# Kernel optimization log

Measured on AMD Instinct MI355X. Metric: run time of the kernel, lower is better.

## Reference

```python
import jax, jax.numpy as jnp
import numpy as np


def setup_inputs() -> dict:
    key = jax.random.key(0)
    k1, k2, k3, k4 = jax.random.split(key, 4)
    B, I, P, F = 4096, 1024, 512, 2048
    x = jax.random.normal(k1, (B, I), dtype=jnp.float32)
    # params initialized like torch.rand(...)*2-1 (uniform in [-1,1])
    features = jax.random.uniform(k2, (F, I), dtype=jnp.float32, minval=-1.0, maxval=1.0)
    prototypes = jax.random.uniform(k3, (P, I), dtype=jnp.float32, minval=-1.0, maxval=1.0)
    # scalars: torch inits to zeros; use small nonzero values so output/grads are informative
    abt = jax.random.normal(k4, (3,), dtype=jnp.float32) * 0.1
    alpha = abt[0:1]
    beta = abt[1:2]
    theta = abt[2:3]
    return {"x": x, "features": features, "prototypes": prototypes,
            "alpha": alpha, "beta": beta, "theta": theta}


def reference(x, features, prototypes, alpha, beta, theta):
    # x: [b, i], features: [f, i], prototypes: [p, i]
    # Original einsums broadcast over p but the projection is p-independent:
    xf = x @ features.T            # [b, f]
    pf = prototypes @ features.T   # [p, f]
    x_pres = jax.nn.relu(xf)       # [b, f]
    p_pres = jax.nn.relu(pf)       # [p, f]
    # common[b,p]       = sum_f xf*pf*relu(xf)*relu(pf)
    # x_distinct[b,p]   = sum_f xf*relu(xf)*(1-relu(pf))
    # p_distinct[b,p]   = sum_f pf*relu(pf)*(1-relu(xf))
    a = xf * x_pres                # [b, f]
    c = pf * p_pres                # [p, f]
    common = a @ c.T                                   # [b, p]
    x_distinctive = a @ (1.0 - p_pres).T               # [b, p]
    p_distinctive = (1.0 - x_pres) @ c.T               # [b, p]
    return theta * common - alpha * x_distinctive - beta * p_distinctive
```

## Files before the change

kernel.cpp:

```cpp
#include <hip/hip_runtime.h>
#include <cstdint>

typedef __attribute__((ext_vector_type(8))) short bf16x8;
typedef __attribute__((ext_vector_type(16))) float f32x16;
typedef __attribute__((ext_vector_type(4))) float f4;
typedef __attribute__((ext_vector_type(8))) unsigned short u16x8;
typedef unsigned short u16;


__device__ __forceinline__ u16 f2bf(float f) {
  uint32_t u = __builtin_bit_cast(uint32_t, f);
  u += 0x7fffu + ((u >> 16) & 1u);
  return (u16)(u >> 16);
}

__device__ __forceinline__ float bf2f(u16 h) {
  return __builtin_bit_cast(float, (uint32_t)h << 16);
}

__device__ __forceinline__ void async_cp16(const void* g, void* l) {
  __builtin_amdgcn_global_load_lds(
      (const __attribute__((address_space(1))) uint32_t*)g,
      (__attribute__((address_space(3))) uint32_t*)l, 16, 0, 0);
}

__global__ __launch_bounds__(256) void cast3(
    const float* __restrict__ x, const float* __restrict__ f,
    const float* __restrict__ p, u16* __restrict__ dst,
    int n1, int n2, int n3) {
  int i = (blockIdx.x * 256 + threadIdx.x) * 8;
  const float* src;
  int local;
  if (i < n1) { src = x; local = i; }
  else if (i < n1 + n2) { src = f; local = i - n1; }
  else if (i < n1 + n2 + n3) { src = p; local = i - n1 - n2; }
  else return;
  f4 a = *(const f4*)(src + local);
  f4 b = *(const f4*)(src + local + 4);
  u16x8 o;
  o[0] = f2bf(a.x); o[1] = f2bf(a.y); o[2] = f2bf(a.z); o[3] = f2bf(a.w);
  o[4] = f2bf(b.x); o[5] = f2bf(b.y); o[6] = f2bf(b.z); o[7] = f2bf(b.w);
  *(u16x8*)(dst + i) = o;
}


__device__ __forceinline__ void stage_tile512(
    const u16* __restrict__ A, const u16* __restrict__ B, int K,
    int k0, int tid, u16* L) {
  const int wave = tid >> 6;
  #pragma unroll
  for (int it = 0; it < 2; ++it) {
    int c = it * 512 + tid;
    int row = c >> 3, pc = c & 7;
    int gc = pc ^ (row & 7);
    async_cp16(A + (size_t)row * K + (k0 + gc * 8),
               &L[(it * 512 + wave * 64) * 8]);
  }
  #pragma unroll
  for (int it = 0; it < 2; ++it) {
    int c = it * 512 + tid;
    int row = c >> 3, pc = c & 7;
    int gc = pc ^ (row & 7);
    async_cp16(B + (size_t)row * K + (k0 + gc * 8),
               &L[8192 + (it * 512 + wave * 64) * 8]);
  }
}

__device__ __forceinline__ void compute_tile512(
    const u16* L, int lane, int wrow, int wcol, f32x16 (&acc)[2]) {
  #pragma unroll
  for (int s = 0; s < 4; ++s) {
    const int h = s * 2 + (lane >> 5);
    const int ra = wrow * 32 + (lane & 31);
    bf16x8 afr = *(const bf16x8*)&L[(ra * 8 + (h ^ (ra & 7))) * 8];
    #pragma unroll
    for (int j = 0; j < 2; ++j) {
      const int rb = wcol * 64 + j * 32 + (lane & 31);
      bf16x8 bfr = *(const bf16x8*)&L[8192 + (rb * 8 + (h ^ (rb & 7))) * 8];
      acc[j] = __builtin_amdgcn_mfma_f32_32x32x16_bf16(afr, bfr, acc[j], 0, 0, 0);
    }
  }
}

__device__ __forceinline__ void mainloop512(
    const u16* __restrict__ A, const u16* __restrict__ B, int K,
    int kbeg, int kend, int tid, u16* lds, f32x16 (&acc)[2]) {
  constexpr int BK = 64;
  constexpr int BUF = 16384;
  const int lane = tid & 63;
  const int wave = tid >> 6;
  const int wrow = wave >> 1, wcol = wave & 1;

  stage_tile512(A, B, K, kbeg, tid, lds);
  int cur = 0;
  for (int k0 = kbeg; k0 < kend; k0 += BK) {
    if (k0 + BK < kend) {
      stage_tile512(A, B, K, k0 + BK, tid, lds + (cur ^ 1) * BUF);
      asm volatile("s_waitcnt vmcnt(4)" ::: "memory");
    } else {
      asm volatile("s_waitcnt vmcnt(0)" ::: "memory");
    }
    __builtin_amdgcn_s_barrier();
    compute_tile512(lds + cur * BUF, lane, wrow, wcol, acc);
    __builtin_amdgcn_s_barrier();
    cur ^= 1;
  }
}


__global__ __launch_bounds__(512) void gemm12(
    const u16* __restrict__ xb, const u16* __restrict__ pb,
    const u16* __restrict__ fb, u16* __restrict__ Acat, u16* __restrict__ Bcat,
    const float* __restrict__ alpha, const float* __restrict__ beta,
    const float* __restrict__ theta) {
  constexpr int TM = 128, K = 1024, N = 2048;
  constexpr int TSTRIDE = 136;
  __shared__ u16 lds[32768];

  const int tid = threadIdx.x;
  const int lane = tid & 63;
  const int wave = tid >> 6;
  const int wrow = wave >> 1, wcol = wave & 1;

  const int bid = blockIdx.x;
  const int xcd = bid & 7, slot = bid >> 3;
  const int xt = (xcd & 3) * 9 + (slot >> 3);
  const int yt = (xcd >> 2) * 8 + (slot & 7);

  const int bm_all = xt * TM;
  const int bn = yt * 128;
  const bool is_x = bm_all < 4096;
  const u16* A = is_x ? xb + (size_t)bm_all * K : pb + (size_t)(bm_all - 4096) * K;
  const u16* B = fb + (size_t)bn * K;

  f32x16 acc[2] = {};
  mainloop512(A, B, K, 0, K, tid, lds, acc);

  float th = 0.f, al = 0.f, be = 0.f;
  if (!is_x) { th = theta[0]; al = alpha[0]; be = beta[0]; }
  u16* dst = is_x ? Acat : Bcat;
  const int rowbase = is_x ? bm_all : bm_all - 4096;
  const int rquad = 4 * (lane >> 5);

  #pragma unroll
  for (int half = 0; half < 2; ++half) {
    __syncthreads();
    #pragma unroll
    for (int j = 0; j < 2; ++j) {
      const int cl = wcol * 64 + j * 32 + (lane & 31);
      #pragma unroll
      for (int r = 0; r < 16; ++r) {
        const int rl = wrow * 32 + (r & 3) + 8 * (r >> 2) + rquad;
        float v = acc[j][r];
        float pres = v > 0.f ? v : 0.f;
        float o;
        if (is_x) o = half == 0 ? v * pres : 1.f - pres;
        else {
          float cc = v * pres;
          o = half == 0 ? th * cc - al * (1.f - pres) : -be * cc;
        }
        lds[rl * TSTRIDE + cl] = f2bf(o);
      }
    }
    __syncthreads();
    #pragma unroll
    for (int v = 0; v < 4; ++v) {
      const int rl = v * 32 + (tid >> 4);
      const int c8 = (tid & 15) * 8;
      u16x8 vec = *(const u16x8*)&lds[rl * TSTRIDE + c8];
      *(u16x8*)&dst[(size_t)(rowbase + rl) * (2 * N) + bn + c8 + half * N] = vec;
    }
  }
}

__global__ __launch_bounds__(512) void gemm3(
    const u16* __restrict__ Acat, const u16* __restrict__ Bcat,
    u16* __restrict__ part) {
  constexpr int TM = 128, TN = 128, K = 4096, KSPLIT = 4;
  __shared__ u16 lds[32768];

  const int tid = threadIdx.x;

  const int bid = blockIdx.x;
  const int xcd = bid & 7, slot = bid >> 3;
  const int bz = xcd >> 1;
  const int bxt = (xcd & 1) * 16 + (slot >> 2);
  const int byt = slot & 3;

  const int bm = bxt * TM;
  const int bn = byt * TN;
  const int kbeg = bz * (K / KSPLIT);
  const int kend = kbeg + (K / KSPLIT);

  f32x16 acc[2] = {};
  mainloop512(Acat + (size_t)bm * K, Bcat + (size_t)bn * K, K, kbeg, kend,
              tid, lds, acc);

  const size_t pbase = ((size_t)bz * 128 + byt * 32 + bxt) * 16384;
  #pragma unroll
  for (int j = 0; j < 2; ++j)
    #pragma unroll
    for (int h = 0; h < 2; ++h) {
      u16x8 o;
      #pragma unroll
      for (int e = 0; e < 8; ++e) o[e] = f2bf(acc[j][h * 8 + e]);
      *(u16x8*)&part[pbase + (size_t)(j * 2 + h) * 4096 + tid * 8] = o;
    }
}

__global__ __launch_bounds__(512) void reduce4(
    const u16* __restrict__ part, float* __restrict__ out) {
  constexpr int N = 512;
  const int tid = threadIdx.x;
  const int lane = tid & 63;
  const int wave = tid >> 6;
  const int wrow = wave >> 1, wcol = wave & 1;
  const int tileId = blockIdx.x >> 2;
  const int q = blockIdx.x & 3;
  const int bm = (tileId & 31) * 128;
  const int bn = (tileId >> 5) * 128;

  float v[8] = {};
  #pragma unroll
  for (int z = 0; z < 4; ++z) {
    u16x8 u = *(const u16x8*)&part[((size_t)z * 128 + tileId) * 16384 +
                                   (size_t)q * 4096 + tid * 8];
    #pragma unroll
    for (int e = 0; e < 8; ++e) v[e] += bf2f(u[e]);
  }
  const int j = q >> 1, h = q & 1;
  const int gc = bn + wcol * 64 + j * 32 + (lane & 31);
  const int grb = bm + wrow * 32 + 4 * (lane >> 5);
  #pragma unroll
  for (int e = 0; e < 8; ++e) {
    const int reg = h * 8 + e;
    out[(size_t)(grb + (reg & 3) + 8 * (reg >> 2)) * N + gc] = v[e];
  }
}

extern "C" void kernel_launch(void* const* d_in, const int* in_sizes, int n_in,
                              void* d_out, int out_size, void* d_ws, size_t ws_size,
                              hipStream_t stream) {
  const float* x     = (const float*)d_in[0];
  const float* feat  = (const float*)d_in[1];
  const float* proto = (const float*)d_in[2];
  const float* alpha = (const float*)d_in[3];
  const float* beta  = (const float*)d_in[4];
  const float* theta = (const float*)d_in[5];
  float* out = (float*)d_out;

  constexpr int Bb = 4096, Ii = 1024, Pp = 512, Ff = 2048;

  char* ws = (char*)d_ws;
  u16* xb   = (u16*)ws;
  u16* fb   = xb + (size_t)Bb * Ii;
  u16* pb   = fb + (size_t)Ff * Ii;
  size_t r0 = 33554432;
  u16* Acat = (u16*)(ws + r0);
  u16* Bcat = Acat + (size_t)Bb * 2 * Ff;
  u16* part = Bcat + (size_t)Pp * 2 * Ff;

  const int n1 = Bb * Ii, n2 = Ff * Ii, n3 = Pp * Ii;
  cast3<<<((n1 + n2 + n3) / 8 + 255) / 256, 256, 0, stream>>>(
      x, feat, proto, xb, n1, n2, n3);

  gemm12<<<576, 512, 0, stream>>>(xb, pb, fb, Acat, Bcat, alpha, beta, theta);

  gemm3<<<512, 512, 0, stream>>>(Acat, Bcat, part);

  reduce4<<<512, 512, 0, stream>>>(part, out);
}
```

Measured before the change: 134.9 us.

## Use 1024-thread blocks with one 32x32 MFMA tile per wave

Doubles the block size from 8 to 16 waves for both GEMMs and the reduction. Each wave now computes a single 32x32 accumulator instead of two, and staging issues one async copy per operand per thread instead of two. The aim is more waves to hide latency, but each wave reuses its A fragment less (one MFMA per A load instead of two), so LDS read traffic per FLOP rises and barriers cover more waves.

Result: slower. 142.1 us (+5.3%).

```diff
diff --git a/kernel.cpp b/kernel.cpp
--- a/kernel.cpp
+++ b/kernel.cpp
@@ -44,71 +44,66 @@
 }
 
 
-__device__ __forceinline__ void stage_tile512(
+__device__ __forceinline__ void stage_tile1k(
     const u16* __restrict__ A, const u16* __restrict__ B, int K,
     int k0, int tid, u16* L) {
   const int wave = tid >> 6;
-  #pragma unroll
-  for (int it = 0; it < 2; ++it) {
-    int c = it * 512 + tid;
+  {
+    int c = tid;
     int row = c >> 3, pc = c & 7;
     int gc = pc ^ (row & 7);
     async_cp16(A + (size_t)row * K + (k0 + gc * 8),
-               &L[(it * 512 + wave * 64) * 8]);
-  }
-  #pragma unroll
-  for (int it = 0; it < 2; ++it) {
-    int c = it * 512 + tid;
+               &L[(wave * 64) * 8]);
+  }
+  {
+    int c = tid;
     int row = c >> 3, pc = c & 7;
     int gc = pc ^ (row & 7);
     async_cp16(B + (size_t)row * K + (k0 + gc * 8),
-               &L[8192 + (it * 512 + wave * 64) * 8]);
-  }
-}
-
-__device__ __forceinline__ void compute_tile512(
-    const u16* L, int lane, int wrow, int wcol, f32x16 (&acc)[2]) {
+               &L[8192 + (wave * 64) * 8]);
+  }
+}
+
+__device__ __forceinline__ void compute_tile1k(
+    const u16* L, int lane, int wrow, int wcol, f32x16& acc) {
   #pragma unroll
   for (int s = 0; s < 4; ++s) {
     const int h = s * 2 + (lane >> 5);
     const int ra = wrow * 32 + (lane & 31);
+    const int rb = wcol * 32 + (lane & 31);
     bf16x8 afr = *(const bf16x8*)&L[(ra * 8 + (h ^ (ra & 7))) * 8];
-    #pragma unroll
-    for (int j = 0; j < 2; ++j) {
-      const int rb = wcol * 64 + j * 32 + (lane & 31);
-      bf16x8 bfr = *(const bf16x8*)&L[8192 + (rb * 8 + (h ^ (rb & 7))) * 8];
-      acc[j] = __builtin_amdgcn_mfma_f32_32x32x16_bf16(afr, bfr, acc[j], 0, 0, 0);
-    }
-  }
-}
-
-__device__ __forceinline__ void mainloop512(
+    bf16x8 bfr = *(const bf16x8*)&L[8192 + (rb * 8 + (h ^ (rb & 7))) * 8];
+    acc = __builtin_amdgcn_mfma_f32_32x32x16_bf16(afr, bfr, acc, 0, 0, 0);
+  }
+}
+
+__device__ __forceinline__ void mainloop1k(
     const u16* __restrict__ A, const u16* __restrict__ B, int K,
-    int kbeg, int kend, int tid, u16* lds, f32x16 (&acc)[2]) {
+    int kbeg, int kend, int tid, u16* lds, f32x16& acc) {
   constexpr int BK = 64;
   constexpr int BUF = 16384;
   const int lane = tid & 63;
   const int wave = tid >> 6;
-  const int wrow = wave >> 1, wcol = wave & 1;
-
-  stage_tile512(A, B, K, kbeg, tid, lds);
+  const int wrow = wave >> 2, wcol = wave & 3;
+
+  stage_tile1k(A, B, K, kbeg, tid, lds);
   int cur = 0;
   for (int k0 = kbeg; k0 < kend; k0 += BK) {
     if (k0 + BK < kend) {
-      stage_tile512(A, B, K, k0 + BK, tid, lds + (cur ^ 1) * BUF);
-      asm volatile("s_waitcnt vmcnt(4)" ::: "memory");
+      stage_tile1k(A, B, K, k0 + BK, tid, lds + (cur ^ 1) * BUF);
+      asm volatile("s_waitcnt vmcnt(2)" ::: "memory");
     } else {
       asm volatile("s_waitcnt vmcnt(0)" ::: "memory");
     }
     __builtin_amdgcn_s_barrier();
-    compute_tile512(lds + cur * BUF, lane, wrow, wcol, acc);
+    compute_tile1k(lds + cur * BUF, lane, wrow, wcol, acc);
     __builtin_amdgcn_s_barrier();
     cur ^= 1;
   }
 }
 
 
-__global__ __launch_bounds__(512) void gemm12(
+__global__ __launch_bounds__(1024) void gemm12(
     const u16* __restrict__ xb, const u16* __restrict__ pb,
     const u16* __restrict__ fb, u16* __restrict__ Acat, u16* __restrict__ Bcat,
     const float* __restrict__ alpha, const float* __restrict__ beta,
@@ -120,7 +115,7 @@
   const int tid = threadIdx.x;
   const int lane = tid & 63;
   const int wave = tid >> 6;
-  const int wrow = wave >> 1, wcol = wave & 1;
+  const int wrow = wave >> 2, wcol = wave & 3;
 
   const int bid = blockIdx.x;
   const int xcd = bid & 7, slot = bid >> 3;
@@ -133,39 +128,36 @@
   const u16* A = is_x ? xb + (size_t)bm_all * K : pb + (size_t)(bm_all - 4096) * K;
   const u16* B = fb + (size_t)bn * K;
 
-  f32x16 acc[2] = {};
-  mainloop512(A, B, K, 0, K, tid, lds, acc);
+  f32x16 acc = {};
+  mainloop1k(A, B, K, 0, K, tid, lds, acc);
 
   float th = 0.f, al = 0.f, be = 0.f;
   if (!is_x) { th = theta[0]; al = alpha[0]; be = beta[0]; }
   u16* dst = is_x ? Acat : Bcat;
   const int rowbase = is_x ? bm_all : bm_all - 4096;
   const int rquad = 4 * (lane >> 5);
+  const int cl = wcol * 32 + (lane & 31);
 
   #pragma unroll
   for (int half = 0; half < 2; ++half) {
     __syncthreads();
     #pragma unroll
-    for (int j = 0; j < 2; ++j) {
-      const int cl = wcol * 64 + j * 32 + (lane & 31);
-      #pragma unroll
-      for (int r = 0; r < 16; ++r) {
-        const int rl = wrow * 32 + (r & 3) + 8 * (r >> 2) + rquad;
-        float v = acc[j][r];
-        float pres = v > 0.f ? v : 0.f;
-        float o;
-        if (is_x) o = half == 0 ? v * pres : 1.f - pres;
-        else {
-          float cc = v * pres;
-          o = half == 0 ? th * cc - al * (1.f - pres) : -be * cc;
-        }
-        lds[rl * TSTRIDE + cl] = f2bf(o);
+    for (int r = 0; r < 16; ++r) {
+      const int rl = wrow * 32 + (r & 3) + 8 * (r >> 2) + rquad;
+      float v = acc[r];
+      float pres = v > 0.f ? v : 0.f;
+      float o;
+      if (is_x) o = half == 0 ? v * pres : 1.f - pres;
+      else {
+        float cc = v * pres;
+        o = half == 0 ? th * cc - al * (1.f - pres) : -be * cc;
       }
+      lds[rl * TSTRIDE + cl] = f2bf(o);
     }
     __syncthreads();
     #pragma unroll
-    for (int v = 0; v < 4; ++v) {
-      const int rl = v * 32 + (tid >> 4);
+    for (int v = 0; v < 2; ++v) {
+      const int rl = v * 64 + (tid >> 4);
       const int c8 = (tid & 15) * 8;
       u16x8 vec = *(const u16x8*)&lds[rl * TSTRIDE + c8];
       *(u16x8*)&dst[(size_t)(rowbase + rl) * (2 * N) + bn + c8 + half * N] = vec;
@@ -173,7 +165,7 @@
   }
 }
 
-__global__ __launch_bounds__(512) void gemm3(
+__global__ __launch_bounds__(1024) void gemm3(
     const u16* __restrict__ Acat, const u16* __restrict__ Bcat,
     u16* __restrict__ part) {
   constexpr int TM = 128, TN = 128, K = 4096, KSPLIT = 4;
@@ -192,31 +184,29 @@
   const int kbeg = bz * (K / KSPLIT);
   const int kend = kbeg + (K / KSPLIT);
 
-  f32x16 acc[2] = {};
-  mainloop512(Acat + (size_t)bm * K, Bcat + (size_t)bn * K, K, kbeg, kend,
-              tid, lds, acc);
+  f32x16 acc = {};
+  mainloop1k(Acat + (size_t)bm * K, Bcat + (size_t)bn * K, K, kbeg, kend,
+             tid, lds, acc);
 
   const size_t pbase = ((size_t)bz * 128 + byt * 32 + bxt) * 16384;
   #pragma unroll
-  for (int j = 0; j < 2; ++j)
-    #pragma unroll
-    for (int h = 0; h < 2; ++h) {
-      u16x8 o;
-      #pragma unroll
-      for (int e = 0; e < 8; ++e) o[e] = f2bf(acc[j][h * 8 + e]);
-      *(u16x8*)&part[pbase + (size_t)(j * 2 + h) * 4096 + tid * 8] = o;
-    }
-}
-
-__global__ __launch_bounds__(512) void reduce4(
+  for (int h = 0; h < 2; ++h) {
+    u16x8 o;
+    #pragma unroll
+    for (int e = 0; e < 8; ++e) o[e] = f2bf(acc[h * 8 + e]);
+    *(u16x8*)&part[pbase + (size_t)h * 8192 + tid * 8] = o;
+  }
+}
+
+__global__ __launch_bounds__(1024) void reduce4(
     const u16* __restrict__ part, float* __restrict__ out) {
   constexpr int N = 512;
   const int tid = threadIdx.x;
   const int lane = tid & 63;
   const int wave = tid >> 6;
-  const int wrow = wave >> 1, wcol = wave & 1;
-  const int tileId = blockIdx.x >> 2;
-  const int q = blockIdx.x & 3;
+  const int wrow = wave >> 2, wcol = wave & 3;
+  const int tileId = blockIdx.x >> 1;
+  const int q = blockIdx.x & 1;
   const int bm = (tileId & 31) * 128;
   const int bn = (tileId >> 5) * 128;
 
@@ -224,16 +214,15 @@
   #pragma unroll
   for (int z = 0; z < 4; ++z) {
     u16x8 u = *(const u16x8*)&part[((size_t)z * 128 + tileId) * 16384 +
-                                   (size_t)q * 4096 + tid * 8];
+                                   (size_t)q * 8192 + tid * 8];
     #pragma unroll
     for (int e = 0; e < 8; ++e) v[e] += bf2f(u[e]);
   }
-  const int j = q >> 1, h = q & 1;
-  const int gc = bn + wcol * 64 + j * 32 + (lane & 31);
+  const int gc = bn + wcol * 32 + (lane & 31);
   const int grb = bm + wrow * 32 + 4 * (lane >> 5);
   #pragma unroll
   for (int e = 0; e < 8; ++e) {
-    const int reg = h * 8 + e;
+    const int reg = q * 8 + e;
     out[(size_t)(grb + (reg & 3) + 8 * (reg >> 2)) * N + gc] = v[e];
   }
 }
@@ -264,9 +253,9 @@
   cast3<<<((n1 + n2 + n3) / 8 + 255) / 256, 256, 0, stream>>>(
       x, feat, proto, xb, n1, n2, n3);
 
-  gemm12<<<576, 512, 0, stream>>>(xb, pb, fb, Acat, Bcat, alpha, beta, theta);
-
-  gemm3<<<512, 512, 0, stream>>>(Acat, Bcat, part);
-
-  reduce4<<<512, 512, 0, stream>>>(part, out);
-}
+  gemm12<<<576, 1024, 0, stream>>>(xb, pb, fb, Acat, Bcat, alpha, beta, theta);
+
+  gemm3<<<512, 1024, 0, stream>>>(Acat, Bcat, part);
+
+  reduce4<<<256, 1024, 0, stream>>>(part, out);
+}
```
